# Optimization experiments

Hardware: AMD Instinct MI355X
Metric: run time of the kernel (lower is better)

The kernel has to match this reference:

```python
import jax, jax.numpy as jnp
import numpy as np

B, N, C, K3, KNN = 4, 4096, 128, 3, 16
SCALE = 1.0 / np.sqrt(C)  # attention uses sqrt(embed_dim)
EPS = 1e-5


def _knn_idx(x, k):
    # squared euclidean distances (monotone in cdist), topk smallest
    x2 = jnp.sum(x * x, axis=-1)                       # [B,N]
    d2 = x2[:, :, None] + x2[:, None, :] - 2.0 * jnp.einsum('bnd,bmd->bnm', x, x)
    _, idx = jax.lax.top_k(-d2, k)                     # [B,N,k]
    return idx


def _gather(x, idx):
    # knn_gather: x [B,N,D], idx [B,N,k] -> [B,N,k,D]
    return jax.vmap(lambda xb, ib: xb[ib])(x, idx)


def _attn(q_in, kv_in, Wq, Wk, Wv):
    # q_in [B,N,D], kv_in [B,N,k,D]; torch Linear: x @ W.T
    Q = q_in @ Wq.T
    Kt = kv_in @ Wk.T
    V = kv_in @ Wv.T
    scores = jnp.einsum('bnkd,bnd->bnk', Kt, Q) * SCALE
    a = jax.nn.softmax(scores, axis=-1)
    return jnp.einsum('bnk,bnkd->bnd', a, V)


def _ln(x, g, b):
    mu = jnp.mean(x, axis=-1, keepdims=True)
    var = jnp.mean((x - mu) ** 2, axis=-1, keepdims=True)
    return (x - mu) * jax.lax.rsqrt(var + EPS) * g + b


def setup_inputs() -> dict:
    key = jax.random.key(0)
    ks = jax.random.split(key, 20)
    s = 0.05
    inp = {
        'src': jax.random.normal(ks[0], (B, N, K3), dtype=jnp.float32),
        'tgt': jax.random.normal(ks[1], (B, N, C), dtype=jnp.float32),
        'Wq0': jax.random.normal(ks[2], (C, C), dtype=jnp.float32) * s,
        'Wk0': jax.random.normal(ks[3], (C, C), dtype=jnp.float32) * s,
        'Wv0': jax.random.normal(ks[4], (C, C), dtype=jnp.float32) * s,
        'Wq1': jax.random.normal(ks[5], (C, C), dtype=jnp.float32) * s,
        'Wk1': jax.random.normal(ks[6], (C, C), dtype=jnp.float32) * s,
        'Wv1': jax.random.normal(ks[7], (C, C), dtype=jnp.float32) * s,
        'Wp0': jax.random.normal(ks[8], (C, K3), dtype=jnp.float32) * s,
        'bp0': jnp.zeros((C,), dtype=jnp.float32),
        'Wp1': jax.random.normal(ks[9], (C, C), dtype=jnp.float32) * s,
        'bp1': jnp.zeros((C,), dtype=jnp.float32),
        'Wl': jax.random.normal(ks[10], (C, C), dtype=jnp.float32) * s,
        'bl': jnp.zeros((C,), dtype=jnp.float32),
        'g0': jnp.ones((C,), dtype=jnp.float32),
        'b0': jnp.zeros((C,), dtype=jnp.float32),
        'g1': jnp.ones((C,), dtype=jnp.float32),
        'b1': jnp.zeros((C,), dtype=jnp.float32),
    }
    return inp


def reference(src, tgt, Wq0, Wk0, Wv0, Wq1, Wk1, Wv1, Wp0, bp0, Wp1, bp1, Wl, bl, g0, b0, g1, b1):
    k = min(KNN, src.shape[1])
    # stage 1: knn on coordinates
    idx = _knn_idx(src, k)
    gather_src = _gather(src, idx)                         # [B,N,k,3]
    residual_src = (src[:, :, None, :] - gather_src) @ Wp0.T + bp0
    gather_tgt = _gather(tgt, idx)                         # [B,N,k,C]
    out = _attn(tgt, residual_src + gather_tgt, Wq0, Wk0, Wv0)
    # stage 2: knn in feature space
    idx2 = _knn_idx(out, k)
    gather_out = _gather(out, idx2)
    residual_out = (out[:, :, None, :] - gather_out) @ Wp1.T + bp1
    out = _attn(out, residual_out + gather_out, Wq1, Wk1, Wv1)
    out_0 = tgt + out
    out_1 = _ln(out_0, g0, b0) @ Wl.T + bl
    out_2 = _ln(tgt + out_1, g1, b1)
    return jnp.transpose(out_2, (1, 0, 2))                 # [N,B,C]
```

## Files before the change

### kernel.cpp

```cpp
#include <hip/hip_runtime.h>
#include <math.h>

#define NB 4
#define NN 4096
#define NC 128
#define NROWS (NB*NN)
#define SCALE_F 0.08838834764831845f

using bf16x8 = __attribute__((ext_vector_type(8))) short;
using f32x4  = __attribute__((ext_vector_type(4))) float;

__device__ __forceinline__ float rl_f(float x, int l) {
    return __int_as_float(__builtin_amdgcn_readlane(__float_as_int(x), l));
}
__device__ __forceinline__ ushort f2bf(float x) {
    unsigned u = __float_as_uint(x);
    return (ushort)((u + 0x7FFF + ((u >> 16) & 1)) >> 16);
}
__device__ __forceinline__ float bf2f(ushort b) { return __uint_as_float(((unsigned)b) << 16); }

__device__ __forceinline__ unsigned long long mkkey(float d2, int idx) {
    unsigned u = __float_as_uint(d2);
    u ^= ((unsigned)((int)u >> 31)) | 0x80000000u;
    return ((unsigned long long)u << 32) | (unsigned)idx;
}

#define DECL16V \
    float v0=INFINITY,v1=INFINITY,v2=INFINITY,v3=INFINITY,v4=INFINITY,v5=INFINITY,v6=INFINITY,v7=INFINITY, \
          v8=INFINITY,v9=INFINITY,v10=INFINITY,v11=INFINITY,v12=INFINITY,v13=INFINITY,v14=INFINITY,v15=INFINITY;

#define INSERT16V(dv) do { float d_=(dv); \
    bool m0=d_<v0,m1=d_<v1,m2=d_<v2,m3=d_<v3,m4=d_<v4,m5=d_<v5,m6=d_<v6,m7=d_<v7, \
         m8=d_<v8,m9=d_<v9,m10=d_<v10,m11=d_<v11,m12=d_<v12,m13=d_<v13,m14=d_<v14,m15=d_<v15; \
    v15=m14?v14:(m15?d_:v15); v14=m13?v13:(m14?d_:v14); v13=m12?v12:(m13?d_:v13); v12=m11?v11:(m12?d_:v12); \
    v11=m10?v10:(m11?d_:v11); v10=m9?v9:(m10?d_:v10); v9 =m8?v8:(m9?d_:v9);  v8 =m7?v7:(m8?d_:v8); \
    v7 =m6?v6:(m7?d_:v7);   v6 =m5?v5:(m6?d_:v6);   v5 =m4?v4:(m5?d_:v5);  v4 =m3?v3:(m4?d_:v4); \
    v3 =m2?v2:(m3?d_:v3);   v2 =m1?v1:(m2?d_:v2);   v1 =m0?v0:(m1?d_:v1);  v0 =m0?d_:v0; } while(0)

#define POP16V(p) do { bool p_=(p); \
    v0=p_?v1:v0; v1=p_?v2:v1; v2=p_?v3:v2; v3=p_?v4:v3; v4=p_?v5:v4; v5=p_?v6:v5; v6=p_?v7:v6; v7=p_?v8:v7; \
    v8=p_?v9:v8; v9=p_?v10:v9; v10=p_?v11:v10; v11=p_?v12:v11; v12=p_?v13:v12; v13=p_?v14:v13; v14=p_?v15:v14; \
    v15=p_?INFINITY:v15; } while(0)

#define KMAX16 0xFFFFFFFFFFFFFFFFull
#define DECL16K \
    unsigned long long K0=KMAX16,K1=KMAX16,K2=KMAX16,K3=KMAX16,K4=KMAX16,K5=KMAX16,K6=KMAX16,K7=KMAX16, \
                       K8=KMAX16,K9=KMAX16,K10=KMAX16,K11=KMAX16,K12=KMAX16,K13=KMAX16,K14=KMAX16,K15=KMAX16;

#define INSERT16K(kv) do { unsigned long long k_=(kv); \
    bool m0=k_<K0,m1=k_<K1,m2=k_<K2,m3=k_<K3,m4=k_<K4,m5=k_<K5,m6=k_<K6,m7=k_<K7, \
         m8=k_<K8,m9=k_<K9,m10=k_<K10,m11=k_<K11,m12=k_<K12,m13=k_<K13,m14=k_<K14,m15=k_<K15; \
    K15=m14?K14:(m15?k_:K15); K14=m13?K13:(m14?k_:K14); K13=m12?K12:(m13?k_:K13); K12=m11?K11:(m12?k_:K12); \
    K11=m10?K10:(m11?k_:K11); K10=m9?K9:(m10?k_:K10);   K9 =m8?K8:(m9?k_:K9);    K8 =m7?K7:(m8?k_:K8); \
    K7 =m6?K6:(m7?k_:K7);     K6 =m5?K5:(m6?k_:K6);     K5 =m4?K4:(m5?k_:K5);    K4 =m3?K3:(m4?k_:K4); \
    K3 =m2?K2:(m3?k_:K3);     K2 =m1?K1:(m2?k_:K2);     K1 =m0?K0:(m1?k_:K1);    K0 =m0?k_:K0; } while(0)

#define POP16K(p) do { bool p_=(p); \
    K0=p_?K1:K0; K1=p_?K2:K1; K2=p_?K3:K2; K3=p_?K4:K3; K4=p_?K5:K4; K5=p_?K6:K5; K6=p_?K7:K6; K7=p_?K8:K7; \
    K8=p_?K9:K8; K9=p_?K10:K9; K10=p_?K11:K10; K11=p_?K12:K11; K12=p_?K13:K12; K13=p_?K14:K13; K14=p_?K15:K14; \
    K15=p_?KMAX16:K15; } while(0)

__global__ void combo_small(const float* __restrict__ Wk0, const float* __restrict__ Wv0,
                            const float* __restrict__ Wp0, const float* __restrict__ bp0,
                            float* __restrict__ WKP0, float* __restrict__ BK0,
                            float* __restrict__ WVP0, float* __restrict__ BV0)
{
    int task = blockIdx.x * 512 + threadIdx.x;
    if (task >= 1024) return;
    int mat = task >> 9; int rem = task & 511;
    int c = rem >> 2, t = rem & 3;
    const float* W = mat ? Wv0 : Wk0;
    float s = 0.f;
    if (t < 3) {
        for (int d = 0; d < 128; ++d) s = fmaf(W[c*128+d], Wp0[d*3+t], s);
        (mat ? WVP0 : WKP0)[c*3+t] = s;
    } else {
        for (int d = 0; d < 128; ++d) s = fmaf(W[c*128+d], bp0[d], s);
        (mat ? BV0 : BK0)[c] = s;
    }
}

__global__ void combo_big(const float* __restrict__ Wk1, const float* __restrict__ Wv1,
                          const float* __restrict__ Wp1, const float* __restrict__ bp1,
                          float* __restrict__ WKD, float* __restrict__ MV1,
                          float* __restrict__ WVD, float* __restrict__ BV1)
{
    int task = blockIdx.x * 256 + threadIdx.x;
    if (task >= 32896) return;
    if (task < 32768) {
        int mat = task >> 14; int rem = task & 16383;
        int c = rem >> 7, tcol = rem & 127;
        const float* W = mat ? Wv1 : Wk1;
        float s = 0.f;
        for (int d = 0; d < 128; ++d) s = fmaf(W[c*128+d], Wp1[d*128+tcol], s);
        if (mat) { MV1[rem] = s; WVD[rem] = Wv1[rem] - s; }
        else     { WKD[rem] = Wk1[rem] - s; }
    } else {
        int c = task - 32768;
        float s = 0.f;
        for (int d = 0; d < 128; ++d) s = fmaf(Wv1[c*128+d], bp1[d], s);
        BV1[c] = s;
    }
}

__global__ void split7(const float* __restrict__ W0, const float* __restrict__ W1,
                       const float* __restrict__ W2, const float* __restrict__ W3,
                       const float* __restrict__ W4, const float* __restrict__ W5,
                       const float* __restrict__ W6,
                       ushort* __restrict__ WSH, ushort* __restrict__ WSL)
{
    int y = blockIdx.y;
    const float* W;
    switch (y) {
        case 0: W = W0; break; case 1: W = W1; break; case 2: W = W2; break;
        case 3: W = W3; break; case 4: W = W4; break; case 5: W = W5; break;
        default: W = W6; break;
    }
    int i = blockIdx.x*256 + threadIdx.x;
    float v = W[i];
    ushort h = f2bf(v);
    WSH[y*16384 + i] = h;
    WSL[y*16384 + i] = f2bf(v - bf2f(h));
}

__global__ void splitx(const float* __restrict__ X, ushort* __restrict__ XH,
                       ushort* __restrict__ XL)
{
    int i = (blockIdx.x*256 + threadIdx.x) * 8;
    float4 a = *(const float4*)&X[i];
    float4 b = *(const float4*)&X[i+4];
    ushort h0=f2bf(a.x),h1=f2bf(a.y),h2=f2bf(a.z),h3=f2bf(a.w);
    ushort h4=f2bf(b.x),h5=f2bf(b.y),h6=f2bf(b.z),h7=f2bf(b.w);
    uint4 ph;
    ph.x=(unsigned)h0|((unsigned)h1<<16); ph.y=(unsigned)h2|((unsigned)h3<<16);
    ph.z=(unsigned)h4|((unsigned)h5<<16); ph.w=(unsigned)h6|((unsigned)h7<<16);
    *(uint4*)&XH[i] = ph;
    ushort l0=f2bf(a.x-bf2f(h0)),l1=f2bf(a.y-bf2f(h1)),l2=f2bf(a.z-bf2f(h2)),l3=f2bf(a.w-bf2f(h3));
    ushort l4=f2bf(b.x-bf2f(h4)),l5=f2bf(b.y-bf2f(h5)),l6=f2bf(b.z-bf2f(h6)),l7=f2bf(b.w-bf2f(h7));
    uint4 pl;
    pl.x=(unsigned)l0|((unsigned)l1<<16); pl.y=(unsigned)l2|((unsigned)l3<<16);
    pl.z=(unsigned)l4|((unsigned)l5<<16); pl.w=(unsigned)l6|((unsigned)l7<<16);
    *(uint4*)&XL[i] = pl;
}

__global__ void srcproj(const float* __restrict__ src, const float* __restrict__ WKP0,
                        const float* __restrict__ WVP0,
                        float* __restrict__ srcKp, float* __restrict__ srcVp)
{
    int gid = blockIdx.x * 256 + threadIdx.x;
    int i = gid >> 7, c = gid & 127;
    float s0 = src[i*3+0], s1 = src[i*3+1], s2 = src[i*3+2];
    srcKp[gid] = fmaf(s0, WKP0[c*3+0], fmaf(s1, WKP0[c*3+1], s2*WKP0[c*3+2]));
    srcVp[gid] = fmaf(s0, WVP0[c*3+0], fmaf(s1, WVP0[c*3+1], s2*WVP0[c*3+2]));
}

__global__ __launch_bounds__(256) void knn1_kernel(const float* __restrict__ src,
                                                   int* __restrict__ idxout)
{
    int lane = threadIdx.x & 63, wave = threadIdx.x >> 6;
    int b7 = blockIdx.x & 7, sub = blockIdx.x >> 3;
    int batch = b7 >> 1;
    int rib = (sub*2 + (b7 & 1))*4 + wave;
    int row = batch*NN + rib;
    const float* sb = src + batch*NN*3;
    float xi0 = sb[rib*3], xi1 = sb[rib*3+1], xi2 = sb[rib*3+2];

    DECL16V
    for (int it = 0; it < 64; ++it) {
        int j = it*64 + lane;
        float dx = xi0 - sb[j*3], dy = xi1 - sb[j*3+1], dz = xi2 - sb[j*3+2];
        float d2 = fmaf(dx, dx, fmaf(dy, dy, dz*dz));
        if (d2 < v15) INSERT16V(d2);
    }
    float T = INFINITY;
    for (int t = 0; t < 16; ++t) {
        float g = v0;
#pragma unroll
        for (int off = 1; off < 64; off <<= 1) g = fminf(g, __shfl_xor(g, off, 64));
        unsigned long long b = __ballot(v0 == g);
        int f = __ffsll((long long)b) - 1;
        POP16V(lane == f);
        T = g;
    }
    unsigned long long below_mask = (lane == 63) ? 0x7fffffffffffffffull : ((1ull << lane) - 1ull);
    int base = 0;
    for (int it = 0; it < 64; ++it) {
        int j = it*64 + lane;
        float dx = xi0 - sb[j*3], dy = xi1 - sb[j*3+1], dz = xi2 - sb[j*3+2];
        float d2 = fmaf(dx, dx, fmaf(dy, dy, dz*dz));
        unsigned long long blt = __ballot(d2 < T);
        if (d2 < T) idxout[row*16 + base + __popcll(blt & below_mask)] = j;
        base += __popcll(blt);
    }
    for (int it = 0; it < 64 && base < 16; ++it) {
        int j = it*64 + lane;
        float dx = xi0 - sb[j*3], dy = xi1 - sb[j*3+1], dz = xi2 - sb[j*3+2];
        float d2 = fmaf(dx, dx, fmaf(dy, dy, dz*dz));
        unsigned long long beq = __ballot(d2 == T);
        int bel = __popcll(beq & below_mask);
        if (d2 == T && base + bel < 16) idxout[row*16 + base + bel] = j;
        base += __popcll(beq);
    }
}

__global__ __launch_bounds__(256, 2) void gemm128(
    const ushort* __restrict__ XHg, const ushort* __restrict__ XLg,
    const ushort* __restrict__ WHb, const ushort* __restrict__ WLb,
    const float* __restrict__ S1, const float* __restrict__ S2,
    float* __restrict__ Ybase)
{
    __shared__ __align__(16) ushort WHs[128*128];
    __shared__ __align__(16) ushort WLs[128*128];
    int tid = threadIdx.x, lane = tid & 63, wave = tid >> 6;
    int y = blockIdx.y;
    const ushort* WH = WHb + y*16384;
    const ushort* WL = WLb + y*16384;
    float* Y = Ybase + (size_t)y*2097152;
    const float* S = (y == 1) ? S1 : ((y == 2) ? S2 : nullptr);
#pragma unroll
    for (int i = 0; i < 8; ++i) {
        int q = tid + 256*i;
        int c = q >> 4, d8 = q & 15;
        int widx = c*128 + ((d8*8) ^ ((c & 7) << 3));
        *(uint4*)&WHs[widx] = *(const uint4*)&WH[c*128 + d8*8];
        *(uint4*)&WLs[widx] = *(const uint4*)&WL[c*128 + d8*8];
    }
    int r = blockIdx.x*64 + wave*16 + (lane & 15);
    int dbase = (lane >> 4) * 8;
    bf16x8 AH[4], AL[4];
#pragma unroll
    for (int ks = 0; ks < 4; ++ks) {
        AH[ks] = *(const bf16x8*)&XHg[(size_t)r*128 + ks*32 + dbase];
        AL[ks] = *(const bf16x8*)&XLg[(size_t)r*128 + ks*32 + dbase];
    }
    __syncthreads();
    int rbase = blockIdx.x*64 + wave*16 + (lane >> 4)*4;
#pragma unroll
    for (int cb = 0; cb < 8; ++cb) {
        int cB = cb*16 + (lane & 15);
        f32x4 acc = {0.f, 0.f, 0.f, 0.f};
#pragma unroll
        for (int ks = 0; ks < 4; ++ks) {
            int bidx = cB*128 + ((ks*32 + dbase) ^ ((cB & 7) << 3));
            bf16x8 bh = *(const bf16x8*)&WHs[bidx];
            bf16x8 bl = *(const bf16x8*)&WLs[bidx];
            acc = __builtin_amdgcn_mfma_f32_16x16x32_bf16(AH[ks], bh, acc, 0, 0, 0);
            acc = __builtin_amdgcn_mfma_f32_16x16x32_bf16(AL[ks], bh, acc, 0, 0, 0);
            acc = __builtin_amdgcn_mfma_f32_16x16x32_bf16(AH[ks], bl, acc, 0, 0, 0);
        }
#pragma unroll
        for (int r2 = 0; r2 < 4; ++r2) {
            int rA = rbase + r2;
            float o = acc[r2];
            if (S) o -= S[(size_t)rA*128 + cB];
            Y[(size_t)rA*128 + cB] = o;
        }
    }
}

__global__ __launch_bounds__(512) void attn_kernel(
    const float* __restrict__ Q,  const float* __restrict__ GK, const float* __restrict__ GV,
    const float* __restrict__ BASE, const float* __restrict__ bv,
    const int* __restrict__ idx, float* __restrict__ outp, float* __restrict__ x2out,
    ushort* __restrict__ xh, ushort* __restrict__ xl)
{
    int tid = threadIdx.x;
    int lane = tid & 63, wave = tid >> 6;
    int xcd = blockIdx.x & 7, sub = blockIdx.x >> 3;
    int batch = xcd >> 1;
    int band = sub*2 + (xcd & 1);
    int rgrp = lane >> 4;
    int dimg = lane & 15;
    int rib = band*32 + wave*4 + rgrp;
    int row = batch*NN + rib;
    int d0 = dimg*8;
    int gbase = lane & 48;
    const float* GKb = GK + (size_t)batch*NN*NC;
    const float* GVb = GV + (size_t)batch*NN*NC;

    float4 q0 = *(const float4*)&Q[(size_t)row*NC + d0];
    float4 q1 = *(const float4*)&Q[(size_t)row*NC + d0 + 4];
    int jv = idx[row*16 + dimg];

    float sc[16];
#pragma unroll
    for (int k = 0; k < 16; ++k) {
        int j = __shfl(jv, gbase + k, 64);
        const float* gk = &GKb[(size_t)j*NC + d0];
        float4 g0 = *(const float4*)gk;
        float4 g1 = *(const float4*)(gk + 4);
        float p = fmaf(q0.x, g0.x, fmaf(q0.y, g0.y, fmaf(q0.z, g0.z, fmaf(q0.w, g0.w,
                  fmaf(q1.x, g1.x, fmaf(q1.y, g1.y, fmaf(q1.z, g1.z, q1.w*g1.w)))))));
#pragma unroll
        for (int off = 1; off < 16; off <<= 1) p += __shfl_xor(p, off, 64);
        sc[k] = p * SCALE_F;
    }
    float m = sc[0];
#pragma unroll
    for (int k = 1; k < 16; ++k) m = fmaxf(m, sc[k]);
    float wsum = 0.f, w[16];
#pragma unroll
    for (int k = 0; k < 16; ++k) { w[k] = expf(sc[k] - m); wsum += w[k]; }
    float inv = 1.f / wsum;

    float4 a0 = {0.f,0.f,0.f,0.f}, a1 = {0.f,0.f,0.f,0.f};
#pragma unroll
    for (int k = 0; k < 16; ++k) {
        int j = __shfl(jv, gbase + k, 64);
        const float* gv = &GVb[(size_t)j*NC + d0];
        float4 v0 = *(const float4*)gv;
        float4 v1 = *(const float4*)(gv + 4);
        float a = w[k] * inv;
        a0.x = fmaf(a, v0.x, a0.x); a0.y = fmaf(a, v0.y, a0.y);
        a0.z = fmaf(a, v0.z, a0.z); a0.w = fmaf(a, v0.w, a0.w);
        a1.x = fmaf(a, v1.x, a1.x); a1.y = fmaf(a, v1.y, a1.y);
        a1.z = fmaf(a, v1.z, a1.z); a1.w = fmaf(a, v1.w, a1.w);
    }
    float4 b0 = *(const float4*)&BASE[(size_t)row*NC + d0];
    float4 b1 = *(const float4*)&BASE[(size_t)row*NC + d0 + 4];
    float4 c0 = *(const float4*)&bv[d0];
    float4 c1 = *(const float4*)&bv[d0 + 4];
    a0.x += b0.x + c0.x; a0.y += b0.y + c0.y; a0.z += b0.z + c0.z; a0.w += b0.w + c0.w;
    a1.x += b1.x + c1.x; a1.y += b1.y + c1.y; a1.z += b1.z + c1.z; a1.w += b1.w + c1.w;
    *(float4*)&outp[(size_t)row*NC + d0]     = a0;
    *(float4*)&outp[(size_t)row*NC + d0 + 4] = a1;

    if (x2out != nullptr) {
        float x2 = fmaf(a0.x, a0.x, fmaf(a0.y, a0.y, fmaf(a0.z, a0.z, fmaf(a0.w, a0.w,
                   fmaf(a1.x, a1.x, fmaf(a1.y, a1.y, fmaf(a1.z, a1.z, a1.w*a1.w)))))));
#pragma unroll
        for (int off = 1; off < 16; off <<= 1) x2 += __shfl_xor(x2, off, 64);
        if (dimg == 0) x2out[row] = x2;
    }
    if (xh != nullptr) {
        ushort h0 = f2bf(a0.x), h1 = f2bf(a0.y), h2 = f2bf(a0.z), h3 = f2bf(a0.w);
        ushort h4 = f2bf(a1.x), h5 = f2bf(a1.y), h6 = f2bf(a1.z), h7 = f2bf(a1.w);
        uint4 ph;
        ph.x = (unsigned)h0 | ((unsigned)h1 << 16);
        ph.y = (unsigned)h2 | ((unsigned)h3 << 16);
        ph.z = (unsigned)h4 | ((unsigned)h5 << 16);
        ph.w = (unsigned)h6 | ((unsigned)h7 << 16);
        *(uint4*)&xh[(size_t)row*NC + d0] = ph;
        ushort l0 = f2bf(a0.x - bf2f(h0)), l1 = f2bf(a0.y - bf2f(h1));
        ushort l2 = f2bf(a0.z - bf2f(h2)), l3 = f2bf(a0.w - bf2f(h3));
        ushort l4 = f2bf(a1.x - bf2f(h4)), l5 = f2bf(a1.y - bf2f(h5));
        ushort l6 = f2bf(a1.z - bf2f(h6)), l7 = f2bf(a1.w - bf2f(h7));
        uint4 pl;
        pl.x = (unsigned)l0 | ((unsigned)l1 << 16);
        pl.y = (unsigned)l2 | ((unsigned)l3 << 16);
        pl.z = (unsigned)l4 | ((unsigned)l5 << 16);
        pl.w = (unsigned)l6 | ((unsigned)l7 << 16);
        *(uint4*)&xl[(size_t)row*NC + d0] = pl;
    }
}

#define SCAN_STEP(CP, X2S, REFRESH) do { \
    float4 dd = *(const float4*)&DT[dtrd]; \
    float4 xx = *(const float4*)&(X2S)[slotl*4]; \
    int cb = 0; \
    { float d2 = fmaf(-2.f, dd.x, xx.x); bool p = d2 <= Trow; \
      unsigned long long bal = __ballot(p); unsigned grp = (unsigned)(bal >> grpsh) & 0xFFFFu; \
      if (p) BUF[srow][cb + __popc(grp & lowm)] = mkkey(d2, (CP) + slotl*4 + 0); \
      cb += __popc(grp); } \
    { float d2 = fmaf(-2.f, dd.y, xx.y); bool p = d2 <= Trow; \
      unsigned long long bal = __ballot(p); unsigned grp = (unsigned)(bal >> grpsh) & 0xFFFFu; \
      if (p) BUF[srow][cb + __popc(grp & lowm)] = mkkey(d2, (CP) + slotl*4 + 1); \
      cb += __popc(grp); } \
    { float d2 = fmaf(-2.f, dd.z, xx.z); bool p = d2 <= Trow; \
      unsigned long long bal = __ballot(p); unsigned grp = (unsigned)(bal >> grpsh) & 0xFFFFu; \
      if (p) BUF[srow][cb + __popc(grp & lowm)] = mkkey(d2, (CP) + slotl*4 + 2); \
      cb += __popc(grp); } \
    { float d2 = fmaf(-2.f, dd.w, xx.w); bool p = d2 <= Trow; \
      unsigned long long bal = __ballot(p); unsigned grp = (unsigned)(bal >> grpsh) & 0xFFFFu; \
      if (p) BUF[srow][cb + __popc(grp & lowm)] = mkkey(d2, (CP) + slotl*4 + 3); \
      cb += __popc(grp); } \
    _Pragma("unroll") \
    for (int r = 0; r < 4; ++r) { \
        int ii = r*16 + slotl; \
        if (ii < cb) { \
            unsigned long long k = BUF[srow][ii]; \
            if (k < K15) INSERT16K(k); \
        } \
    } \
    if (REFRESH) { \
        unsigned long long tk = K15; \
        _Pragma("unroll") \
        for (int off = 1; off < 16; off <<= 1) { \
            unsigned long long o = __shfl_xor(tk, off, 64); \
            tk = (o < tk) ? o : tk; \
        } \
        unsigned uu = (unsigned)(tk >> 32); \
        uu = (uu > 0xFF800000u) ? 0xFF800000u : uu; \
        uu = (uu & 0x80000000u) ? (uu ^ 0x80000000u) : ~uu; \
        Trow = __uint_as_float(uu); \
    } \
} while (0)

__global__ __launch_bounds__(512, 2) void knn2_kernel(const ushort* __restrict__ XHg,
                                                      const ushort* __restrict__ XLg,
                                                      const float* __restrict__ x2g,
                                                      int* __restrict__ idxout)
{
    __shared__ __align__(16) ushort XCH[64*128];
    __shared__ __align__(16) ushort XCL[64*128];
    __shared__ __align__(16) float  DT[32*64];
    __shared__ unsigned long long   BUF[32][65];
    __shared__ __align__(16) float  X2T[2][64];
    int tid = threadIdx.x;
    int lane = tid & 63, wave = tid >> 6;
    int xcd = blockIdx.x & 7, sub = blockIdx.x >> 3;
    int batch = xcd >> 1;
    int band = sub*2 + (xcd & 1);
    const ushort* XHb = XHg + (size_t)batch*NN*NC;
    const ushort* XLb = XLg + (size_t)batch*NN*NC;
    const float*  x2b = x2g + (size_t)batch*NN;
    int r0 = band*32;

    int rowblk = wave & 1, colblk = wave >> 1;
    int dbase = (lane >> 4) * 8;
    int gr = r0 + rowblk*16 + (lane & 15);
    bf16x8 AH[4], AL[4];
#pragma unroll
    for (int ks = 0; ks < 4; ++ks) {
        AH[ks] = *(const bf16x8*)&XHb[(size_t)gr*NC + ks*32 + dbase];
        AL[ks] = *(const bf16x8*)&XLb[(size_t)gr*NC + ks*32 + dbase];
    }
    int cB = colblk*16 + (lane & 15);
    int colw = colblk*16 + (lane & 15);

    int srow = tid >> 4, slotl = tid & 15;
    int grpsh = lane & 48;
    unsigned lowm = (1u << slotl) - 1u;
    int dtrd = srow*64 + ((slotl*4 + 4*srow) & 63);
    float Trow = INFINITY;
    DECL16K

    for (int t = 0; t < 64; ++t) {
        int c0 = t*64;
        __syncthreads();
#pragma unroll
        for (int i = 0; i < 2; ++i) {
            int qq = tid + 512*i;
            int c = qq >> 4, d8 = qq & 15;
            int widx = c*128 + ((d8*8) ^ ((c & 7) << 3));
            *(uint4*)&XCH[widx] = *(const uint4*)&XHb[(size_t)(c0 + c)*NC + d8*8];
            *(uint4*)&XCL[widx] = *(const uint4*)&XLb[(size_t)(c0 + c)*NC + d8*8];
        }
        if (tid < 64) X2T[t & 1][tid] = x2b[c0 + tid];
        if (t > 0) {
            const float* x2s = X2T[(t - 1) & 1];
            SCAN_STEP(c0 - 64, x2s, 1);
        }
        __syncthreads();
        f32x4 acc = {0.f, 0.f, 0.f, 0.f};
#pragma unroll
        for (int ks = 0; ks < 4; ++ks) {
            int bidx = cB*128 + ((ks*32 + dbase) ^ ((cB & 7) << 3));
            bf16x8 bh = *(const bf16x8*)&XCH[bidx];
            bf16x8 bl = *(const bf16x8*)&XCL[bidx];
            acc = __builtin_amdgcn_mfma_f32_16x16x32_bf16(AH[ks], bh, acc, 0, 0, 0);
            acc = __builtin_amdgcn_mfma_f32_16x16x32_bf16(AL[ks], bh, acc, 0, 0, 0);
            acc = __builtin_amdgcn_mfma_f32_16x16x32_bf16(AH[ks], bl, acc, 0, 0, 0);
        }
#pragma unroll
        for (int r2 = 0; r2 < 4; ++r2) {
            int rA = rowblk*16 + (lane >> 4)*4 + r2;
            DT[rA*64 + (((colw & ~3) + 4*rA) & 63) + (colw & 3)] = acc[r2];
        }
    }
    __syncthreads();
    {
        const float* x2s = X2T[1];
        SCAN_STEP(63*64, x2s, 0);
    }
    int grow = batch*NN + r0 + srow;
    for (int tt = 0; tt < 16; ++tt) {
        unsigned long long g = K0;
#pragma unroll
        for (int off = 1; off < 16; off <<= 1) {
            unsigned long long o = __shfl_xor(g, off, 64);
            g = (o < g) ? o : g;
        }
        bool win = (K0 == g);
        if (win) idxout[grow*16 + tt] = (int)(unsigned)(g & 0xFFFFFFFFull);
        POP16K(win);
    }
}

__global__ __launch_bounds__(256) void final_kernel(
    const float* __restrict__ tgt, const float* __restrict__ att,
    const float* __restrict__ Wl, const float* __restrict__ bl,
    const float* __restrict__ g0, const float* __restrict__ b0,
    const float* __restrict__ g1, const float* __restrict__ b1,
    float* __restrict__ outp)
{
    __shared__ float WL[128*128];
    int tid = threadIdx.x;
    for (int f = tid; f < 16384; f += 256) {
        int c = f >> 7, d = f & 127;
        WL[d*128 + (c ^ (d & 14))] = Wl[f];
    }
    __syncthreads();
    int lane = tid & 63, wave = tid >> 6;
    float2 gg0 = *(const float2*)&g0[2*lane];
    float2 bb0 = *(const float2*)&b0[2*lane];
    float2 gg1 = *(const float2*)&g1[2*lane];
    float2 bb1 = *(const float2*)&b1[2*lane];
    float2 bl2 = *(const float2*)&bl[2*lane];
    for (int it = 0; it < 4; ++it) {
        int row0 = blockIdx.x*64 + it*16 + wave*4;
        float2 tg[4];
        float lnx[4], lny[4];
#pragma unroll
        for (int r = 0; r < 4; ++r) {
            int row = row0 + r;
            tg[r] = *(const float2*)&tgt[row*128 + 2*lane];
            float2 at = *(const float2*)&att[row*128 + 2*lane];
            float ox = tg[r].x + at.x, oy = tg[r].y + at.y;
            float s = ox + oy;
#pragma unroll
            for (int off = 1; off < 64; off <<= 1) s += __shfl_xor(s, off, 64);
            float mu = s * (1.f/128.f);
            float dx = ox - mu, dy = oy - mu;
            float vv = fmaf(dx, dx, dy*dy);
#pragma unroll
            for (int off = 1; off < 64; off <<= 1) vv += __shfl_xor(vv, off, 64);
            float rstd = rsqrtf(vv * (1.f/128.f) + 1e-5f);
            lnx[r] = dx * rstd * gg0.x + bb0.x;
            lny[r] = dy * rstd * gg0.y + bb0.y;
        }
        float2 acc[4];
#pragma unroll
        for (int r = 0; r < 4; ++r) { acc[r].x = 0.f; acc[r].y = 0.f; }
#pragma unroll 8
        for (int dh = 0; dh < 64; ++dh) {
            int cidx = (2*lane) ^ ((2*dh) & 14);
            float2 wa = *(const float2*)&WL[(2*dh)*128 + cidx];
            float2 wb = *(const float2*)&WL[(2*dh+1)*128 + cidx];
#pragma unroll
            for (int r = 0; r < 4; ++r) {
                float xa = rl_f(lnx[r], dh);
                float xb = rl_f(lny[r], dh);
                acc[r].x = fmaf(xa, wa.x, acc[r].x);
                acc[r].y = fmaf(xa, wa.y, acc[r].y);
                acc[r].x = fmaf(xb, wb.x, acc[r].x);
                acc[r].y = fmaf(xb, wb.y, acc[r].y);
            }
        }
#pragma unroll
        for (int r = 0; r < 4; ++r) {
            int row = row0 + r;
            float zx = tg[r].x + acc[r].x + bl2.x;
            float zy = tg[r].y + acc[r].y + bl2.y;
            float s = zx + zy;
#pragma unroll
            for (int off = 1; off < 64; off <<= 1) s += __shfl_xor(s, off, 64);
            float mu = s * (1.f/128.f);
            float dx = zx - mu, dy = zy - mu;
            float vv = fmaf(dx, dx, dy*dy);
#pragma unroll
            for (int off = 1; off < 64; off <<= 1) vv += __shfl_xor(vv, off, 64);
            float rstd = rsqrtf(vv * (1.f/128.f) + 1e-5f);
            float2 res;
            res.x = dx * rstd * gg1.x + bb1.x;
            res.y = dy * rstd * gg1.y + bb1.y;
            int b = row >> 12, n = row & 4095;
            *(float2*)&outp[((size_t)n*NB + b)*128 + 2*lane] = res;
        }
    }
}

extern "C" void kernel_launch(void* const* d_in, const int* in_sizes, int n_in,
                              void* d_out, int out_size, void* d_ws, size_t ws_size,
                              hipStream_t stream)
{
    (void)in_sizes; (void)n_in; (void)out_size; (void)ws_size;
    const float* src = (const float*)d_in[0];
    const float* tgt = (const float*)d_in[1];
    const float* Wq0 = (const float*)d_in[2];
    const float* Wk0 = (const float*)d_in[3];
    const float* Wv0 = (const float*)d_in[4];
    const float* Wq1 = (const float*)d_in[5];
    const float* Wk1 = (const float*)d_in[6];
    const float* Wv1 = (const float*)d_in[7];
    const float* Wp0 = (const float*)d_in[8];
    const float* bp0 = (const float*)d_in[9];
    const float* Wp1 = (const float*)d_in[10];
    const float* bp1 = (const float*)d_in[11];
    const float* Wl  = (const float*)d_in[12];
    const float* bl  = (const float*)d_in[13];
    const float* g0  = (const float*)d_in[14];
    const float* b0  = (const float*)d_in[15];
    const float* g1  = (const float*)d_in[16];
    const float* b1  = (const float*)d_in[17];
    float* out = (float*)d_out;

    float* A0   = (float*)d_ws;
    float* A1   = A0 + 2097152;
    float* A2   = A1 + 2097152;
    float* A3   = A2 + 2097152;
    float* A4   = A3 + 2097152;
    float* OUT1 = A4 + 2097152;
    int*   IDX1 = (int*)(OUT1 + 2097152);
    int*   IDX2 = IDX1 + NROWS*16;
    float* X2G  = (float*)(IDX2 + NROWS*16);
    float* WKP0 = X2G + NROWS;
    float* BK0  = WKP0 + 384;
    float* WVP0 = BK0 + 128;
    float* BV0  = WVP0 + 384;
    float* WKD  = BV0 + 128;
    float* MV1  = WKD + 16384;
    float* WVD  = MV1 + 16384;
    float* BV1  = WVD + 16384;
    ushort* WSH = (ushort*)(BV1 + 128);
    ushort* WSL = WSH + 7*16384;
    ushort* XH  = WSL + 7*16384;
    ushort* XL  = XH + (size_t)NROWS*NC;

    combo_small<<<dim3(2), dim3(512), 0, stream>>>(Wk0, Wv0, Wp0, bp0, WKP0, BK0, WVP0, BV0);
    combo_big<<<dim3(129), dim3(256), 0, stream>>>(Wk1, Wv1, Wp1, bp1, WKD, MV1, WVD, BV1);
    split7<<<dim3(64, 7), dim3(256), 0, stream>>>(Wq0, Wk0, Wv0, Wq1, WKD, WVD, MV1, WSH, WSL);
    srcproj<<<dim3(8192), dim3(256), 0, stream>>>(src, WKP0, WVP0, A3, A4);
    splitx<<<dim3(1024), dim3(256), 0, stream>>>(tgt, XH, XL);
    knn1_kernel<<<dim3(4096), dim3(256), 0, stream>>>(src, IDX1);
    gemm128<<<dim3(256, 3), dim3(256), 0, stream>>>(XH, XL, WSH, WSL, A3, A4, A0);
    attn_kernel<<<dim3(512), dim3(512), 0, stream>>>(A0, A1, A2, A4, BV0, IDX1, OUT1, X2G, XH, XL);
    knn2_kernel<<<dim3(512), dim3(512), 0, stream>>>(XH, XL, X2G, IDX2);
    gemm128<<<dim3(256, 4), dim3(256), 0, stream>>>(XH, XL, WSH + 3*16384, WSL + 3*16384,
                                                    nullptr, nullptr, A0);
    attn_kernel<<<dim3(512), dim3(512), 0, stream>>>(A0, A1, A2, A3, BV1, IDX2, OUT1, nullptr, nullptr, nullptr);
    final_kernel<<<dim3(256), dim3(256), 0, stream>>>(tgt, OUT1, Wl, bl, g0, b0, g1, b1, out);
}
```

Before: 428.4 us.

## Split feature-space KNN over column halves with merge kernel and wave-skip scan

Each knn2 block now scans only half of the candidate columns, so twice as many blocks run, and each writes a partial sorted top-16 key list. A new merge kernel combines the two partial lists into the final indices. The candidate scan skips all buffer work when no lane in a wave passes the threshold, and falls back to direct inserts when a row's buffer would overflow. The low-part bf16 tile is no longer staged in LDS but read straight from global memory, and launch bounds ask for higher occupancy. The cost is an extra launch, a partial-key buffer that aliases A0, and more global traffic for the low-part operand.

```diff
diff --git a/kernel.cpp b/kernel.cpp
--- a/kernel.cpp
+++ b/kernel.cpp
@@ -357,29 +357,37 @@
 #define SCAN_STEP(CP, X2S, REFRESH) do { \
     float4 dd = *(const float4*)&DT[dtrd]; \
     float4 xx = *(const float4*)&(X2S)[slotl*4]; \
-    int cb = 0; \
-    { float d2 = fmaf(-2.f, dd.x, xx.x); bool p = d2 <= Trow; \
-      unsigned long long bal = __ballot(p); unsigned grp = (unsigned)(bal >> grpsh) & 0xFFFFu; \
-      if (p) BUF[srow][cb + __popc(grp & lowm)] = mkkey(d2, (CP) + slotl*4 + 0); \
-      cb += __popc(grp); } \
-    { float d2 = fmaf(-2.f, dd.y, xx.y); bool p = d2 <= Trow; \
-      unsigned long long bal = __ballot(p); unsigned grp = (unsigned)(bal >> grpsh) & 0xFFFFu; \
-      if (p) BUF[srow][cb + __popc(grp & lowm)] = mkkey(d2, (CP) + slotl*4 + 1); \
-      cb += __popc(grp); } \
-    { float d2 = fmaf(-2.f, dd.z, xx.z); bool p = d2 <= Trow; \
-      unsigned long long bal = __ballot(p); unsigned grp = (unsigned)(bal >> grpsh) & 0xFFFFu; \
-      if (p) BUF[srow][cb + __popc(grp & lowm)] = mkkey(d2, (CP) + slotl*4 + 2); \
-      cb += __popc(grp); } \
-    { float d2 = fmaf(-2.f, dd.w, xx.w); bool p = d2 <= Trow; \
-      unsigned long long bal = __ballot(p); unsigned grp = (unsigned)(bal >> grpsh) & 0xFFFFu; \
-      if (p) BUF[srow][cb + __popc(grp & lowm)] = mkkey(d2, (CP) + slotl*4 + 3); \
-      cb += __popc(grp); } \
-    _Pragma("unroll") \
-    for (int r = 0; r < 4; ++r) { \
-        int ii = r*16 + slotl; \
-        if (ii < cb) { \
-            unsigned long long k = BUF[srow][ii]; \
-            if (k < K15) INSERT16K(k); \
+    float d2q0 = fmaf(-2.f, dd.x, xx.x); \
+    float d2q1 = fmaf(-2.f, dd.y, xx.y); \
+    float d2q2 = fmaf(-2.f, dd.z, xx.z); \
+    float d2q3 = fmaf(-2.f, dd.w, xx.w); \
+    bool p0 = d2q0 <= Trow, p1 = d2q1 <= Trow, p2 = d2q2 <= Trow, p3 = d2q3 <= Trow; \
+    if (__ballot(p0 | p1 | p2 | p3)) { \
+        unsigned g0 = (unsigned)(__ballot(p0) >> grpsh) & 0xFFFFu; \
+        unsigned g1 = (unsigned)(__ballot(p1) >> grpsh) & 0xFFFFu; \
+        unsigned g2 = (unsigned)(__ballot(p2) >> grpsh) & 0xFFFFu; \
+        unsigned g3 = (unsigned)(__ballot(p3) >> grpsh) & 0xFFFFu; \
+        int c0n = __popc(g0), c1n = __popc(g1), c2n = __popc(g2), c3n = __popc(g3); \
+        int total = c0n + c1n + c2n + c3n; \
+        if (total <= 32) { \
+            if (p0) BUF[srow][__popc(g0 & lowm)]             = mkkey(d2q0, (CP) + slotl*4 + 0); \
+            if (p1) BUF[srow][c0n + __popc(g1 & lowm)]       = mkkey(d2q1, (CP) + slotl*4 + 1); \
+            if (p2) BUF[srow][c0n + c1n + __popc(g2 & lowm)] = mkkey(d2q2, (CP) + slotl*4 + 2); \
+            if (p3) BUF[srow][c0n + c1n + c2n + __popc(g3 & lowm)] = mkkey(d2q3, (CP) + slotl*4 + 3); \
+            if (slotl < total) { \
+                unsigned long long k = BUF[srow][slotl]; \
+                if (k < K15) INSERT16K(k); \
+            } \
+            if (16 + slotl < total) { \
+                unsigned long long k = BUF[srow][16 + slotl]; \
+                if (k < K15) INSERT16K(k); \
+            } \
+        } else { \
+            unsigned long long kq; \
+            if (p0) { kq = mkkey(d2q0, (CP) + slotl*4 + 0); if (kq < K15) INSERT16K(kq); } \
+            if (p1) { kq = mkkey(d2q1, (CP) + slotl*4 + 1); if (kq < K15) INSERT16K(kq); } \
+            if (p2) { kq = mkkey(d2q2, (CP) + slotl*4 + 2); if (kq < K15) INSERT16K(kq); } \
+            if (p3) { kq = mkkey(d2q3, (CP) + slotl*4 + 3); if (kq < K15) INSERT16K(kq); } \
         } \
     } \
     if (REFRESH) { \
@@ -396,25 +404,26 @@
     } \
 } while (0)
 
-__global__ __launch_bounds__(512, 2) void knn2_kernel(const ushort* __restrict__ XHg,
+__global__ __launch_bounds__(512, 8) void knn2_kernel(const ushort* __restrict__ XHg,
                                                       const ushort* __restrict__ XLg,
                                                       const float* __restrict__ x2g,
-                                                      int* __restrict__ idxout)
+                                                      unsigned long long* __restrict__ kpart)
 {
     __shared__ __align__(16) ushort XCH[64*128];
-    __shared__ __align__(16) ushort XCL[64*128];
     __shared__ __align__(16) float  DT[32*64];
-    __shared__ unsigned long long   BUF[32][65];
+    __shared__ unsigned long long   BUF[32][33];
     __shared__ __align__(16) float  X2T[2][64];
     int tid = threadIdx.x;
     int lane = tid & 63, wave = tid >> 6;
-    int xcd = blockIdx.x & 7, sub = blockIdx.x >> 3;
+    int b = blockIdx.x;
+    int xcd = b & 7, half = (b >> 3) & 1, sub = b >> 4;
     int batch = xcd >> 1;
     int band = sub*2 + (xcd & 1);
     const ushort* XHb = XHg + (size_t)batch*NN*NC;
     const ushort* XLb = XLg + (size_t)batch*NN*NC;
     const float*  x2b = x2g + (size_t)batch*NN;
     int r0 = band*32;
+    int cbase = half*2048;
 
     int rowblk = wave & 1, colblk = wave >> 1;
     int dbase = (lane >> 4) * 8;
@@ -426,7 +435,7 @@
         AL[ks] = *(const bf16x8*)&XLb[(size_t)gr*NC + ks*32 + dbase];
     }
     int cB = colblk*16 + (lane & 15);
-    int colw = colblk*16 + (lane & 15);
+    int colw = cB;
 
     int srow = tid >> 4, slotl = tid & 15;
     int grpsh = lane & 48;
@@ -435,8 +444,8 @@
     float Trow = INFINITY;
     DECL16K
 
-    for (int t = 0; t < 64; ++t) {
-        int c0 = t*64;
+    for (int t = 0; t < 32; ++t) {
+        int c0 = cbase + t*64;
         __syncthreads();
 #pragma unroll
         for (int i = 0; i < 2; ++i) {
@@ -444,7 +453,6 @@
             int c = qq >> 4, d8 = qq & 15;
             int widx = c*128 + ((d8*8) ^ ((c & 7) << 3));
             *(uint4*)&XCH[widx] = *(const uint4*)&XHb[(size_t)(c0 + c)*NC + d8*8];
-            *(uint4*)&XCL[widx] = *(const uint4*)&XLb[(size_t)(c0 + c)*NC + d8*8];
         }
         if (tid < 64) X2T[t & 1][tid] = x2b[c0 + tid];
         if (t > 0) {
@@ -457,7 +465,7 @@
         for (int ks = 0; ks < 4; ++ks) {
             int bidx = cB*128 + ((ks*32 + dbase) ^ ((cB & 7) << 3));
             bf16x8 bh = *(const bf16x8*)&XCH[bidx];
-            bf16x8 bl = *(const bf16x8*)&XCL[bidx];
+            bf16x8 bl = *(const bf16x8*)&XLb[(size_t)(c0 + cB)*NC + ks*32 + dbase];
             acc = __builtin_amdgcn_mfma_f32_16x16x32_bf16(AH[ks], bh, acc, 0, 0, 0);
             acc = __builtin_amdgcn_mfma_f32_16x16x32_bf16(AL[ks], bh, acc, 0, 0, 0);
             acc = __builtin_amdgcn_mfma_f32_16x16x32_bf16(AH[ks], bl, acc, 0, 0, 0);
@@ -471,7 +479,7 @@
     __syncthreads();
     {
         const float* x2s = X2T[1];
-        SCAN_STEP(63*64, x2s, 0);
+        SCAN_STEP(cbase + 31*64, x2s, 0);
     }
     int grow = batch*NN + r0 + srow;
     for (int tt = 0; tt < 16; ++tt) {
@@ -481,9 +489,24 @@
             unsigned long long o = __shfl_xor(g, off, 64);
             g = (o < g) ? o : g;
         }
-        bool win = (K0 == g);
-        if (win) idxout[grow*16 + tt] = (int)(unsigned)(g & 0xFFFFFFFFull);
-        POP16K(win);
+        if (slotl == 0) kpart[(size_t)grow*32 + half*16 + tt] = g;
+        POP16K(K0 == g);
+    }
+}
+
+__global__ __launch_bounds__(256) void knn2_merge(const unsigned long long* __restrict__ KP,
+                                                  int* __restrict__ idxout)
+{
+    int row = blockIdx.x*256 + threadIdx.x;
+    const unsigned long long* a = &KP[(size_t)row*32];
+    const unsigned long long* bq = a + 16;
+    int ia = 0, ib = 0;
+#pragma unroll
+    for (int t = 0; t < 16; ++t) {
+        unsigned long long ka = a[ia], kb = bq[ib];
+        bool ta = ka < kb;
+        idxout[row*16 + t] = (int)(unsigned)((ta ? ka : kb) & 0xFFFFFFFFull);
+        ia += ta ? 1 : 0; ib += ta ? 0 : 1;
     }
 }
 
@@ -616,6 +639,7 @@
     ushort* WSL = WSH + 7*16384;
     ushort* XH  = WSL + 7*16384;
     ushort* XL  = XH + (size_t)NROWS*NC;
+    unsigned long long* KPART = (unsigned long long*)A0;
 
     combo_small<<<dim3(2), dim3(512), 0, stream>>>(Wk0, Wv0, Wp0, bp0, WKP0, BK0, WVP0, BV0);
     combo_big<<<dim3(129), dim3(256), 0, stream>>>(Wk1, Wv1, Wp1, bp1, WKD, MV1, WVD, BV1);
@@ -625,7 +649,8 @@
     knn1_kernel<<<dim3(4096), dim3(256), 0, stream>>>(src, IDX1);
     gemm128<<<dim3(256, 3), dim3(256), 0, stream>>>(XH, XL, WSH, WSL, A3, A4, A0);
     attn_kernel<<<dim3(512), dim3(512), 0, stream>>>(A0, A1, A2, A4, BV0, IDX1, OUT1, X2G, XH, XL);
-    knn2_kernel<<<dim3(512), dim3(512), 0, stream>>>(XH, XL, X2G, IDX2);
+    knn2_kernel<<<dim3(1024), dim3(512), 0, stream>>>(XH, XL, X2G, KPART);
+    knn2_merge<<<dim3(64), dim3(256), 0, stream>>>(KPART, IDX2);
     gemm128<<<dim3(256, 4), dim3(256), 0, stream>>>(XH, XL, WSH + 3*16384, WSL + 3*16384,
                                                     nullptr, nullptr, A0);
     attn_kernel<<<dim3(512), dim3(512), 0, stream>>>(A0, A1, A2, A3, BV1, IDX2, OUT1, nullptr, nullptr, nullptr);
```

Result: slower. 933.0 us (+117.8%).
